# Optimization experiments

Hardware: AMD Instinct MI355X
Metric: run time of the kernel (lower is better)

## Reference

```python
import jax, jax.numpy as jnp
import numpy as np

EPS = 1e-8
TAU = 1.0


def _spatial_adjacency(segments, n_seg):
    # segments: (B, H, W) int. Counts 4-neighbour pixel adjacencies between segments;
    # diagonal counts pixels per segment (self loops kept).
    B, H, W = segments.shape
    b = jnp.arange(B)[:, None]
    adj = jnp.zeros((B, n_seg, n_seg), jnp.float32)
    flat = segments.reshape(B, -1)
    adj = adj.at[b, flat, flat].add(1.0)  # self loops = segment sizes
    s1 = segments[:, :, :-1].reshape(B, -1)
    s2 = segments[:, :, 1:].reshape(B, -1)
    adj = adj.at[b, s1, s2].add(1.0).at[b, s2, s1].add(1.0)
    v1 = segments[:, :-1, :].reshape(B, -1)
    v2 = segments[:, 1:, :].reshape(B, -1)
    adj = adj.at[b, v1, v2].add(1.0).at[b, v2, v1].add(1.0)
    return adj


def _proximity_adjacency(segments, n_seg):
    adj = _spatial_adjacency(segments, n_seg)
    # zero connections of node 0 except its diagonal
    adj = adj.at[:, 1:, 0].set(0.0).at[:, 0, 1:].set(0.0)
    size_node = jnp.diagonal(adj, axis1=-2, axis2=-1)
    new_diag = adj.sum(axis=2) - size_node + 1.0
    idx = jnp.arange(n_seg)
    adj = adj.at[:, idx, idx].set(new_diag)
    # normalize_adjacency(binarize=True, normalize=False)
    return (adj > 0).astype(jnp.float32)


def setup_inputs() -> dict:
    key = jax.random.key(0)
    k1, k2, k3 = jax.random.split(key, 3)
    B, N, D, R = 8, 2048, 384, 64
    H = W = 256
    x = jax.random.normal(k1, (B, N, D), jnp.float32)
    segments = jax.random.randint(k2, (B, H, W), 0, N, jnp.int64)
    prototypes = jax.random.normal(k3, (1, R, D), jnp.float32)
    return {"x": x, "segments": segments, "prototypes": prototypes}


def reference(x, segments, prototypes):
    B, N, D = x.shape
    prox_adj = _proximity_adjacency(segments, N)  # (B, N, N) binary

    # node-presence mask (B, N)
    b = jnp.arange(B)[:, None]
    flat = segments.reshape(B, -1)
    mask = jnp.zeros((B, N), jnp.float32).at[b, flat].max(1.0)

    # cosine prototype clustering (Q = V = K = Identity)
    protos = prototypes[0]  # (R, D)
    qn = x / jnp.maximum(jnp.linalg.norm(x, axis=-1, keepdims=True), EPS)
    kn = protos / jnp.maximum(jnp.linalg.norm(protos, axis=-1, keepdims=True), EPS)
    Csim = (jnp.einsum('bnd,rd->bnr', qn, kn) + 1.0) * 0.5
    S = Csim / Csim.sum(axis=-1, keepdims=True)  # soft assignment (B, N, R)

    # cluster alignment loss (DEC-style sharpened-target KL, masked over present nodes)
    P = S ** 2 / (S.sum(axis=1, keepdims=True) + EPS)
    P = P / (P.sum(axis=-1, keepdims=True) + EPS)
    kl = (P * (jnp.log(P + EPS) - jnp.log(S + EPS))).sum(axis=-1)  # (B, N)
    loss = (kl * mask).sum() / (mask.sum() + EPS)

    # affinity adjacency from assignments
    C = jax.nn.softmax(S * TAU, axis=-1)  # (B, N, R)
    cn = jnp.linalg.norm(C, axis=-1)  # (B, N)
    proto_adj = jnp.einsum('bnr,bmr->bnm', C, C) / (cn[:, :, None] * cn[:, None, :] + EPS)
    adj = prox_adj * proto_adj
    # normalize_adjacency(normalize=True): row normalization
    adj = adj / (adj.sum(axis=-1, keepdims=True) + EPS)

    out = jnp.einsum('bnm,bmd->bnd', adj, x)  # adj @ values
    return out, segments, loss, C
```

## Files before the change

### kernel.cpp

```cpp
#include <hip/hip_runtime.h>
#include <hip/hip_bf16.h>

#define NB 8
#define NN 2048
#define ND 384
#define NR 64
#define OUT_ELEMS (NB*NN*ND)
#define SEG_ELEMS (NB*256*256)
#define NBLK_LOSS (NB*NN/4)
#define NBCAP 384

typedef float  f32x4  __attribute__((ext_vector_type(4)));
typedef short  bf16x8 __attribute__((ext_vector_type(8)));

__device__ inline float wsum(float v){
  #pragma unroll
  for(int o=32;o;o>>=1) v += __shfl_xor(v,o,64);
  return v;
}
__device__ inline float wmax(float v){
  #pragma unroll
  for(int o=32;o;o>>=1) v = fmaxf(v,__shfl_xor(v,o,64));
  return v;
}
__device__ inline unsigned short f2bf(float f){
  unsigned u = __float_as_uint(f);
  return (unsigned short)((u + 0x8000u) >> 16);
}
__device__ inline float bf2f(short s){
  return __uint_as_float(((unsigned)(unsigned short)s) << 16);
}

__device__ __forceinline__ void gl2lds16(const unsigned short* g, unsigned short* s){
  __builtin_amdgcn_global_load_lds(
      (const __attribute__((address_space(1))) unsigned int*)g,
      (__attribute__((address_space(3))) unsigned int*)s,
      16, 0, 0);
}

__global__ void k_proto(const float* __restrict__ protos, float* __restrict__ kn){
  int r = blockIdx.x, l = threadIdx.x;
  float v[6]; float ss = 0.f;
  #pragma unroll
  for(int i=0;i<6;i++){ v[i] = protos[r*ND + l*6 + i]; ss += v[i]*v[i]; }
  ss = wsum(ss);
  float inv = 1.f / fmaxf(sqrtf(ss), 1e-8f);
  #pragma unroll
  for(int i=0;i<6;i++) kn[r*ND + l*6 + i] = v[i]*inv;
}

__global__ __launch_bounds__(1024) void k_seg(const int* __restrict__ seg,
                                              float* __restrict__ mask,
                                              unsigned* __restrict__ prox){
  __shared__ unsigned lm[64*64];
  int tid = threadIdx.x;
  int b  = blockIdx.x & 7;
  int rg = blockIdx.x >> 3;
  int base = rg << 6;
  for(int i=tid; i<64*64; i+=1024) lm[i] = 0u;
  __syncthreads();
  const int* sb = seg + b*65536;

#define PAIR(S, S2) { \
    if((S) != (S2) && (S) != 0 && (S2) != 0){ \
      if(((S )>>6)==rg) atomicOr(&lm[(((S )&63)<<6) + ((S2)>>5)], 1u<<((S2)&31)); \
      if(((S2)>>6)==rg) atomicOr(&lm[(((S2)&63)<<6) + ((S )>>5)], 1u<<((S )&31)); \
    } }

  #pragma unroll 1
  for(int it=0; it<16; ++it){
    int g = it*1024 + tid;
    int p = g*4;
    int i = g >> 6;
    int j = (g & 63)*4;
    int4 a = *(const int4*)(sb + p);
    if((a.x>>6)==rg) mask[(b<<11) + a.x] = 1.f;
    if((a.y>>6)==rg) mask[(b<<11) + a.y] = 1.f;
    if((a.z>>6)==rg) mask[(b<<11) + a.z] = 1.f;
    if((a.w>>6)==rg) mask[(b<<11) + a.w] = 1.f;
    PAIR(a.x, a.y); PAIR(a.y, a.z); PAIR(a.z, a.w);
    if(j < 252){
      int n = sb[p + 4];
      PAIR(a.w, n);
    }
    if(i < 255){
      int4 v = *(const int4*)(sb + p + 256);
      PAIR(a.x, v.x); PAIR(a.y, v.y); PAIR(a.z, v.z); PAIR(a.w, v.w);
    }
  }
#undef PAIR
  __syncthreads();
  unsigned* dst = prox + ((size_t)(b<<11) + base)*64;
  *(uint4*)(dst + tid*4) = *(const uint4*)&lm[tid*4];
}

__global__ __launch_bounds__(256) void k_csim(const float* __restrict__ x,
                                              const float* __restrict__ kn,
                                              float* __restrict__ Sout,
                                              unsigned short* __restrict__ xTbf,
                                              float* __restrict__ part){
  __shared__ float xT[32*68];
  __shared__ float kT[32*68];
  __shared__ float xinvS[64];
  __shared__ float csh[16*64];
  int t = threadIdx.x;
  int m0 = blockIdx.x * 64;
  float acc[4][4] = {};
  int mload = t>>2, koff = (t&3)*8;
  int mb = (t>>4)*4, rb = (t&15)*4;
  float ssq = 0.f;
  for(int c=0;c<12;c++){
    int k0 = c*32;
    __syncthreads();
    const float4* xg = (const float4*)(x + (size_t)(m0+mload)*ND + k0 + koff);
    float4 a = xg[0], bq = xg[1];
    ssq += a.x*a.x + a.y*a.y + a.z*a.z + a.w*a.w
         + bq.x*bq.x + bq.y*bq.y + bq.z*bq.z + bq.w*bq.w;
    xT[(koff+0)*68+mload]=a.x;  xT[(koff+1)*68+mload]=a.y;  xT[(koff+2)*68+mload]=a.z;  xT[(koff+3)*68+mload]=a.w;
    xT[(koff+4)*68+mload]=bq.x; xT[(koff+5)*68+mload]=bq.y; xT[(koff+6)*68+mload]=bq.z; xT[(koff+7)*68+mload]=bq.w;
    const float4* kg = (const float4*)(kn + mload*ND + k0 + koff);
    float4 ka = kg[0], kb = kg[1];
    kT[(koff+0)*68+mload]=ka.x; kT[(koff+1)*68+mload]=ka.y; kT[(koff+2)*68+mload]=ka.z; kT[(koff+3)*68+mload]=ka.w;
    kT[(koff+4)*68+mload]=kb.x; kT[(koff+5)*68+mload]=kb.y; kT[(koff+6)*68+mload]=kb.z; kT[(koff+7)*68+mload]=kb.w;
    __syncthreads();
    {
      int k2 = t>>3, mo = (t&7)*8;
      const float* src = &xT[k2*68 + mo];
      float4 aa = *(const float4*)src;
      float4 bb = *(const float4*)(src+4);
      uint4 o;
      o.x = (unsigned)f2bf(aa.x) | ((unsigned)f2bf(aa.y)<<16);
      o.y = (unsigned)f2bf(aa.z) | ((unsigned)f2bf(aa.w)<<16);
      o.z = (unsigned)f2bf(bb.x) | ((unsigned)f2bf(bb.y)<<16);
      o.w = (unsigned)f2bf(bb.z) | ((unsigned)f2bf(bb.w)<<16);
      int bb2 = m0 >> 11, ml = m0 & 2047;
      *(uint4*)(xTbf + ((size_t)(bb2*ND + k0 + k2))*NN + ml + mo) = o;
    }
    for(int k=0;k<32;k++){
      float xv[4], kv[4];
      *(float4*)xv = *(const float4*)&xT[k*68+mb];
      *(float4*)kv = *(const float4*)&kT[k*68+rb];
      #pragma unroll
      for(int mi=0;mi<4;mi++)
        #pragma unroll
        for(int ri=0;ri<4;ri++) acc[mi][ri] += xv[mi]*kv[ri];
    }
  }
  ssq += __shfl_xor(ssq,1,64);
  ssq += __shfl_xor(ssq,2,64);
  if((t&3)==0) xinvS[mload] = 1.f / fmaxf(sqrtf(ssq), 1e-8f);
  __syncthreads();
  float sv[4][4];
  #pragma unroll
  for(int mi=0;mi<4;mi++){
    float xin = xinvS[mb+mi];
    float rsum = 0.f;
    #pragma unroll
    for(int ri=0;ri<4;ri++){
      float vv = (acc[mi][ri]*xin + 1.f)*0.5f;
      sv[mi][ri] = vv; rsum += vv;
    }
    rsum += __shfl_xor(rsum,1,64);
    rsum += __shfl_xor(rsum,2,64);
    rsum += __shfl_xor(rsum,4,64);
    rsum += __shfl_xor(rsum,8,64);
    float inv = 1.f/rsum;
    #pragma unroll
    for(int ri=0;ri<4;ri++) sv[mi][ri] *= inv;
    *(float4*)&Sout[(size_t)(m0+mb+mi)*NR + rb] = *(const float4*)sv[mi];
  }
  {
    float4 pc;
    pc.x = sv[0][0]+sv[1][0]+sv[2][0]+sv[3][0];
    pc.y = sv[0][1]+sv[1][1]+sv[2][1]+sv[3][1];
    pc.z = sv[0][2]+sv[1][2]+sv[2][2]+sv[3][2];
    pc.w = sv[0][3]+sv[1][3]+sv[2][3]+sv[3][3];
    *(float4*)&csh[(t>>4)*64 + rb] = pc;
  }
  __syncthreads();
  if(t < 64){
    float a = 0.f;
    #pragma unroll
    for(int g=0;g<16;g++) a += csh[g*64 + t];
    part[(size_t)blockIdx.x*64 + t] = a;
  }
}

__global__ void k_lossfc(float* Smat, const float* __restrict__ part,
                         const float* __restrict__ mask,
                         float* __restrict__ klp, float* __restrict__ mp,
                         unsigned short* __restrict__ Kbf){
  __shared__ float shk[4], shm[4];
  int w = threadIdx.x>>6, l = threadIdx.x&63;
  int node = blockIdx.x*4 + w;
  int b = node >> 11;
  float s = Smat[(size_t)node*NR + l];
  float csm = 0.f;
  #pragma unroll
  for(int c=0;c<32;c++) csm += part[(size_t)((b<<5)+c)*64 + l];
  float p = s*s/(csm + 1e-8f);
  float ps = wsum(p);
  float P = p/(ps + 1e-8f);
  float term = P*(logf(P + 1e-8f) - logf(s + 1e-8f));
  float kl = wsum(term);
  if(l==0){ float mv = mask[node]; shk[w] = kl*mv; shm[w] = mv; }
  float mx = wmax(s);
  float e = expf(s - mx);
  float Z = wsum(e);
  float c = e / Z;
  float cn2 = wsum(c*c);
  Smat[(size_t)node*NR + l] = c;
  Kbf[(size_t)node*NR + l] = f2bf(c * rsqrtf(cn2));
  __syncthreads();
  if(threadIdx.x==0){
    klp[blockIdx.x] = shk[0]+shk[1]+shk[2]+shk[3];
    mp [blockIdx.x] = shm[0]+shm[1]+shm[2]+shm[3];
  }
}

__global__ __launch_bounds__(256) void k_nbr(const unsigned short* __restrict__ Kbf,
                                             const unsigned* __restrict__ prox,
                                             unsigned* __restrict__ nbr,
                                             unsigned short* __restrict__ off){
  int w = threadIdx.x>>6, L = threadIdx.x&63;
  int n = blockIdx.x*4 + w;
  int node = n & (NN-1);
  const unsigned short* KbB = Kbf + ((size_t)(n >> 11))*NN*NR;

  unsigned word = prox[(size_t)n*64 + L];
  if(L == (node>>5)) word |= 1u << (node&31);
  int pc = __popc(word);
  int pre = pc;
  #pragma unroll
  for(int o=1;o<64;o<<=1){
    int v = __shfl_up(pre, o, 64);
    if(L >= o) pre += v;
  }
  int base = pre - pc;
  if((L&1)==0) off[(size_t)n*33 + (L>>1)] = (unsigned short)base;
  if(L==63)    off[(size_t)n*33 + 32]     = (unsigned short)pre;

  const bf16x8* cnp = (const bf16x8*)(Kbf + (size_t)n*NR);
  float cnf[64];
  #pragma unroll
  for(int s=0;s<8;s++){
    bf16x8 cv = cnp[s];
    #pragma unroll
    for(int e=0;e<8;e++) cnf[s*8+e] = bf2f(cv[e]);
  }

  unsigned* nb = nbr + (size_t)n*NBCAP;
  int idx = base;
  while(word){
    int bit = __ffs(word) - 1;
    word &= word - 1;
    int m = (L<<5) + bit;
    const bf16x8* cmp = (const bf16x8*)(KbB + (size_t)m*NR);
    float acc = 0.f;
    #pragma unroll
    for(int s=0;s<8;s++){
      bf16x8 cv = cmp[s];
      #pragma unroll
      for(int e=0;e<8;e++) acc += cnf[s*8+e]*bf2f(cv[e]);
    }
    if(idx < NBCAP) nb[idx] = ((unsigned)m<<16) | (unsigned)f2bf(acc);
    idx++;
  }
}

__global__ __launch_bounds__(256, 3) void k_pv(const unsigned* __restrict__ nbr,
                                               const unsigned short* __restrict__ off,
                                               const unsigned short* __restrict__ xTbf,
                                               float* __restrict__ out){
  __shared__ unsigned short Al[64*64];
  __shared__ unsigned short Bl[128*64];
  __shared__ unsigned short offL[64*33];
  int tid = threadIdx.x;
  int w = tid>>6, l = tid&63, q = l>>4, li = l&15;
  int b  = blockIdx.x & 7;
  int mt = (blockIdx.x>>3) & 31;
  int ct = blockIdx.x >> 8;
  int m0 = mt*64;
  int d0 = ct*128;
  const unsigned short* xTb = xTbf + (size_t)b*ND*NN;

  int wr = w & 1, wc = w >> 1;

  int lrow8 = l>>3;
  int sgel  = ((l&7) ^ lrow8) * 8;
  const unsigned short* gsrc[4];
  unsigned short* ldst[4];
  #pragma unroll
  for(int j=0;j<4;j++){
    int id = w*4 + j;
    ldst[j] = Bl + id*512;
    gsrc[j] = xTb + (size_t)(d0 + id*8 + lrow8)*NN + sgel;
  }

  int srow = tid>>2, g = tid&3;
  int r7s  = srow & 7;
  const unsigned* ebase = nbr + (size_t)(b*NN + m0 + srow)*NBCAP;
  for(int j=g; j<33; j+=4)
    offL[srow*33 + j] = off[(size_t)(b*NN + m0 + srow)*33 + j];

  f32x4 acc[2][4];
  #pragma unroll
  for(int nc=0;nc<2;nc++)
    #pragma unroll
    for(int t=0;t<4;t++) acc[nc][t] = (f32x4)(0.f);
  f32x4 rs[2] = {(f32x4)(0.f),(f32x4)(0.f)};
  bf16x8 ones;
  #pragma unroll
  for(int i=0;i<8;i++) ones[i] = (short)0x3F80;

  int r7 = li & 7;
  for(int k0=0; k0<NN; k0+=64){
    int t = k0 >> 6;
    __syncthreads();
    {
      uint4 z = {0,0,0,0};
      *(uint4*)&Al[tid*16]     = z;
      *(uint4*)&Al[tid*16 + 8] = z;
    }
    __syncthreads();
    #pragma unroll
    for(int j=0;j<4;j++) gl2lds16(gsrc[j] + k0, ldst[j]);
    {
      int s0 = offL[srow*33 + t];
      int s1 = offL[srow*33 + t + 1];
      if(s1 > NBCAP) s1 = NBCAP;
      for(int i=s0+g; i<s1; i+=4){
        unsigned e = ebase[i];
        int col = (int)(e >> 16) - k0;
        int phys = (((col>>3) ^ r7s) << 3) | (col & 7);
        Al[srow*64 + phys] = (unsigned short)(e & 0xffffu);
      }
    }
    __syncthreads();

    #pragma unroll
    for(int s=0;s<2;s++){
      int ps = ((s*4 + q) ^ r7) * 8;
      bf16x8 a0 = *(const bf16x8*)&Al[(wr*32 +      li)*64 + ps];
      bf16x8 a1 = *(const bf16x8*)&Al[(wr*32 + 16 + li)*64 + ps];
      bf16x8 bv[4];
      #pragma unroll
      for(int t2=0;t2<4;t2++)
        bv[t2] = *(const bf16x8*)&Bl[(wc*64 + t2*16 + li)*64 + ps];
      #pragma unroll
      for(int t2=0;t2<4;t2++){
        acc[0][t2] = __builtin_amdgcn_mfma_f32_16x16x32_bf16(a0, bv[t2], acc[0][t2], 0,0,0);
        acc[1][t2] = __builtin_amdgcn_mfma_f32_16x16x32_bf16(a1, bv[t2], acc[1][t2], 0,0,0);
      }
      rs[0] = __builtin_amdgcn_mfma_f32_16x16x32_bf16(a0, ones, rs[0], 0,0,0);
      rs[1] = __builtin_amdgcn_mfma_f32_16x16x32_bf16(a1, ones, rs[1], 0,0,0);
    }
  }

  #pragma unroll
  for(int nc=0;nc<2;nc++)
    #pragma unroll
    for(int r=0;r<4;r++){
      int row = m0 + wr*32 + nc*16 + q*4 + r;
      float inv = 1.f/(rs[nc][r] + 1e-8f);
      float* orow = out + ((size_t)(b*NN + row))*ND + d0 + wc*64;
      #pragma unroll
      for(int t2=0;t2<4;t2++)
        orow[t2*16 + li] = acc[nc][t2][r] * inv;
    }
}

__global__ void k_segout(const int* __restrict__ seg, float* __restrict__ o,
                         const float* __restrict__ klp, const float* __restrict__ mp,
                         float* __restrict__ outLoss){
  int tid = threadIdx.x;
  int i = blockIdx.x*256 + tid;
  o[i] = (float)seg[i];
  if(blockIdx.x==0){
    __shared__ float sa[4], sm[4];
    float a=0.f, m=0.f;
    for(int k=tid; k<NBLK_LOSS; k+=256){ a += klp[k]; m += mp[k]; }
    a = wsum(a); m = wsum(m);
    if((tid&63)==0){ sa[tid>>6]=a; sm[tid>>6]=m; }
    __syncthreads();
    if(tid==0)
      outLoss[0] = (sa[0]+sa[1]+sa[2]+sa[3])/((sm[0]+sm[1]+sm[2]+sm[3])+1e-8f);
  }
}

extern "C" void kernel_launch(void* const* d_in, const int* in_sizes, int n_in,
                              void* d_out, int out_size, void* d_ws, size_t ws_size,
                              hipStream_t stream) {
  const float* x      = (const float*)d_in[0];
  const int*   seg    = (const int*)d_in[1];
  const float* protos = (const float*)d_in[2];

  float* out     = (float*)d_out;
  float* outSeg  = out + OUT_ELEMS;
  float* outLoss = outSeg + SEG_ELEMS;
  float* outC    = outLoss + 1;

  unsigned short* xTbf = (unsigned short*)d_ws;
  unsigned short* Kbf  = xTbf + (size_t)NB*ND*NN;
  unsigned short* Pbf  = Kbf + (size_t)NB*NN*NR;
  unsigned*       nbr  = (unsigned*)Pbf;
  unsigned short* off  = (unsigned short*)(nbr + (size_t)NB*NN*NBCAP);
  float* kn      = (float*)(Pbf + (size_t)NB*NN*NN);
  float* maskp   = kn + NR*ND;
  unsigned* prox = (unsigned*)(maskp + NB*NN);
  float* part    = (float*)(prox + (size_t)NB*NN*64);
  float* klp     = part + NB*32*64;
  float* mp      = klp + NBLK_LOSS;

  hipMemsetAsync(maskp, 0, (size_t)NB*NN*4, stream);

  k_proto <<<dim3(NR),           dim3(64),   0, stream>>>(protos, kn);
  k_seg   <<<dim3(256),          dim3(1024), 0, stream>>>(seg, maskp, prox);
  k_csim  <<<dim3(NB*NN/64),     dim3(256),  0, stream>>>(x, kn, outC, xTbf, part);
  k_lossfc<<<dim3(NBLK_LOSS),    dim3(256),  0, stream>>>(outC, part, maskp, klp, mp, Kbf);
  k_nbr   <<<dim3(NB*NN/4),      dim3(256),  0, stream>>>(Kbf, prox, nbr, off);
  k_pv    <<<dim3(768),          dim3(256),  0, stream>>>(nbr, off, xTbf, out);
  k_segout<<<dim3(SEG_ELEMS/256),dim3(256),  0, stream>>>(seg, outSeg, klp, mp, outLoss);
}
```

Baseline: 269.2 us.

## Compute sparse neighbour affinities with dense MFMA tiles instead of per-lane scalar dots

The old neighbour kernel had each lane walk its set adjacency bits and compute a scalar 64-wide bf16 dot product per neighbour. That gave divergent loops and scattered loads. It is now split into an offset kernel and a new kernel that computes dense 64x64 tiles of C·Cᵀ with bf16 MFMA. Each kernel then writes only the entries the proximity bitmask marks, using popcount-based positions. This swaps irregular scalar work for dense matrix-core work over the whole N×N space, about 16x more FLOPs, plus an extra launch.

```diff
diff --git a/kernel.cpp b/kernel.cpp
--- a/kernel.cpp
+++ b/kernel.cpp
@@ -26,9 +26,6 @@
 __device__ inline unsigned short f2bf(float f){
   unsigned u = __float_as_uint(f);
   return (unsigned short)((u + 0x8000u) >> 16);
-}
-__device__ inline float bf2f(short s){
-  return __uint_as_float(((unsigned)(unsigned short)s) << 16);
 }
 
 __device__ __forceinline__ void gl2lds16(const unsigned short* g, unsigned short* s){
@@ -218,15 +215,11 @@
   }
 }
 
-__global__ __launch_bounds__(256) void k_nbr(const unsigned short* __restrict__ Kbf,
-                                             const unsigned* __restrict__ prox,
-                                             unsigned* __restrict__ nbr,
+__global__ __launch_bounds__(256) void k_off(const unsigned* __restrict__ prox,
                                              unsigned short* __restrict__ off){
   int w = threadIdx.x>>6, L = threadIdx.x&63;
   int n = blockIdx.x*4 + w;
   int node = n & (NN-1);
-  const unsigned short* KbB = Kbf + ((size_t)(n >> 11))*NN*NR;
-
   unsigned word = prox[(size_t)n*64 + L];
   if(L == (node>>5)) word |= 1u << (node&31);
   int pc = __popc(word);
@@ -239,32 +232,73 @@
   int base = pre - pc;
   if((L&1)==0) off[(size_t)n*33 + (L>>1)] = (unsigned short)base;
   if(L==63)    off[(size_t)n*33 + 32]     = (unsigned short)pre;
-
-  const bf16x8* cnp = (const bf16x8*)(Kbf + (size_t)n*NR);
-  float cnf[64];
-  #pragma unroll
-  for(int s=0;s<8;s++){
-    bf16x8 cv = cnp[s];
-    #pragma unroll
-    for(int e=0;e<8;e++) cnf[s*8+e] = bf2f(cv[e]);
-  }
-
-  unsigned* nb = nbr + (size_t)n*NBCAP;
-  int idx = base;
-  while(word){
-    int bit = __ffs(word) - 1;
-    word &= word - 1;
-    int m = (L<<5) + bit;
-    const bf16x8* cmp = (const bf16x8*)(KbB + (size_t)m*NR);
-    float acc = 0.f;
-    #pragma unroll
-    for(int s=0;s<8;s++){
-      bf16x8 cv = cmp[s];
-      #pragma unroll
-      for(int e=0;e<8;e++) acc += cnf[s*8+e]*bf2f(cv[e]);
-    }
-    if(idx < NBCAP) nb[idx] = ((unsigned)m<<16) | (unsigned)f2bf(acc);
-    idx++;
+}
+
+__global__ __launch_bounds__(256) void k_qks(const unsigned short* __restrict__ Kbf,
+                                             const unsigned* __restrict__ prox,
+                                             const unsigned short* __restrict__ off,
+                                             unsigned* __restrict__ nbr){
+  int tid = threadIdx.x;
+  int w = tid>>6, l = tid&63, q = l>>4, li = l&15;
+  int b  = blockIdx.x & 7;
+  int qt = (blockIdx.x>>3) & 31;
+  int kc = blockIdx.x >> 8;
+  const unsigned short* Kb = Kbf + (size_t)b*NN*NR;
+
+  int arow = qt*64 + w*16 + li;
+  bf16x8 af0 = *(const bf16x8*)(Kb + (size_t)arow*NR + q*8);
+  bf16x8 af1 = *(const bf16x8*)(Kb + (size_t)arow*NR + 32 + q*8);
+
+  int base[4];
+  #pragma unroll
+  for(int r=0;r<4;r++)
+    base[r] = off[(size_t)(b*NN + qt*64 + w*16 + q*4 + r)*33 + kc*8];
+
+  unsigned below = (1u<<li) - 1u;
+
+  #pragma unroll 1
+  for(int kt = kc*8; kt < kc*8 + 8; ++kt){
+    uint2 mw[4];
+    #pragma unroll
+    for(int r=0;r<4;r++)
+      mw[r] = *(const uint2*)(prox + ((size_t)(b*NN + qt*64 + w*16 + q*4 + r))*64 + kt*2);
+    if(qt==kt){
+      #pragma unroll
+      for(int r=0;r<4;r++){
+        int lrow = w*16 + q*4 + r;
+        if((lrow>>5)==0) mw[r].x |= 1u<<(lrow&31); else mw[r].y |= 1u<<(lrow&31);
+      }
+    }
+    bf16x8 b0[4], b1[4];
+    #pragma unroll
+    for(int f=0;f<4;f++){
+      const unsigned short* p = Kb + (size_t)(kt*64 + f*16 + li)*NR + q*8;
+      b0[f] = *(const bf16x8*)p;
+      b1[f] = *(const bf16x8*)(p + 32);
+    }
+    f32x4 pacc[4] = {(f32x4)(0.f),(f32x4)(0.f),(f32x4)(0.f),(f32x4)(0.f)};
+    #pragma unroll
+    for(int f=0;f<4;f++){
+      pacc[f] = __builtin_amdgcn_mfma_f32_16x16x32_bf16(af0, b0[f], pacc[f], 0,0,0);
+      pacc[f] = __builtin_amdgcn_mfma_f32_16x16x32_bf16(af1, b1[f], pacc[f], 0,0,0);
+    }
+    #pragma unroll
+    for(int r=0;r<4;r++){
+      unsigned* nrow = nbr + (size_t)(b*NN + qt*64 + w*16 + q*4 + r)*NBCAP;
+      #pragma unroll
+      for(int f=0;f<4;f++){
+        unsigned wd  = (f<2) ? mw[r].x : mw[r].y;
+        unsigned m16 = (wd >> ((f&1)*16)) & 0xFFFFu;
+        if(m16){
+          if((m16 >> li) & 1u){
+            int idx = base[r] + __popc(m16 & below);
+            if(idx < NBCAP)
+              nrow[idx] = ((unsigned)(kt*64 + f*16 + li) << 16) | (unsigned)f2bf(pacc[f][r]);
+          }
+          base[r] += __popc(m16);
+        }
+      }
+    }
   }
 }
 
@@ -418,7 +452,8 @@
   k_seg   <<<dim3(256),          dim3(1024), 0, stream>>>(seg, maskp, prox);
   k_csim  <<<dim3(NB*NN/64),     dim3(256),  0, stream>>>(x, kn, outC, xTbf, part);
   k_lossfc<<<dim3(NBLK_LOSS),    dim3(256),  0, stream>>>(outC, part, maskp, klp, mp, Kbf);
-  k_nbr   <<<dim3(NB*NN/4),      dim3(256),  0, stream>>>(Kbf, prox, nbr, off);
+  k_off   <<<dim3(NB*NN/4),      dim3(256),  0, stream>>>(prox, off);
+  k_qks   <<<dim3(4096),         dim3(256),  0, stream>>>(Kbf, prox, off, nbr);
   k_pv    <<<dim3(768),          dim3(256),  0, stream>>>(nbr, off, xTbf, out);
   k_segout<<<dim3(SEG_ELEMS/256),dim3(256),  0, stream>>>(seg, outSeg, klp, mp, outLoss);
 }
```

After: 583.3 us. 2.17x slower.
